# Performance work log

Measured on AMD Instinct MI355X. Metric: run time of the kernel, lower is better.

Reference implementation:

```python
import math
import jax, jax.numpy as jnp
import numpy as np

B, H, M, L, D, HID = 4, 8, 1024, 3200, 128, 1024
ATTN_LIM, RAMP = 2048, 128
PRE_DIV, LOSS_COEF = 16.0, 1e-06
SIZE = ATTN_LIM  # ExpireSpanDrop size = args.attn_lim


def skew(X, pad_value):
    # X: (BH, M, K) -> (BH, M, K+M), shifting row i right by i (relative-pos trick)
    BH, Mq, K = X.shape
    X = jnp.pad(X, ((0, 0), (0, 0), (0, Mq + 1)), constant_values=pad_value)
    X = X.reshape(BH, -1)[:, :-Mq]
    return X.reshape(BH, Mq, K + Mq)


def setup_inputs():
    key = jax.random.key(0)
    ks = jax.random.split(key, 6)
    query = jax.random.normal(ks[0], (B * H, M, D), jnp.float32)
    k = jax.random.normal(ks[1], (B * H, L, D), jnp.float32)
    v = jax.random.normal(ks[2], (B * H, L, D), jnp.float32)
    memory_hid = jax.random.normal(ks[3], (B, L, HID), jnp.float32)
    # age counters: oldest slot first; the current block (last M slots) goes down to -(M-1)
    memory_counter = jnp.broadcast_to(
        jnp.arange(L - 1, -1, -1, dtype=jnp.float32) - (M - 1), (B, L))
    key_pe = 0.02 * jax.random.normal(ks[4], (1, D, M), jnp.float32)
    span_w = 0.01 * jax.random.normal(ks[5], (1, HID), jnp.float32)
    span_b = jnp.full((1,), -math.log(1.0 / 0.1 - 1.0), jnp.float32)  # init_percentage=0.1
    return {"query": query, "key": k, "value": v, "memory_hid": memory_hid,
            "memory_counter": memory_counter, "key_pe": key_pe,
            "span_w": span_w, "span_b": span_b}


def reference(query, key, value, memory_hid, memory_counter, key_pe, span_w, span_b):
    max_mem = ATTN_LIM + M + RAMP
    # QK^T
    attn = jnp.einsum('bmd,bld->bml', query, key)                              # (BH, M, L)
    # --- ExpireSpanDrop (eval mode, no noise) ---
    max_span = jax.nn.sigmoid(
        jnp.einsum('blh,oh->blo', memory_hid / PRE_DIV, span_w)[..., 0] + span_b[0]) * SIZE  # (B, L)
    remaining_offset = max_span - memory_counter                               # (B, L)
    remaining_span = remaining_offset[:, None, :] - jnp.arange(M, dtype=jnp.float32)[None, :, None]  # (B, M, L)
    emask = jnp.clip(remaining_span / RAMP + 1.0, 0.0, 1.0)
    ramp_mask = ((emask > 0) & (emask < 1)).astype(emask.dtype)
    aux_loss = (remaining_span * ramp_mask).sum((-1, -2)) / RAMP / M * LOSS_COEF  # (B,)
    # causal mask (precomputed buffer in torch)
    causal = jnp.tril(jnp.ones((M, max_mem), jnp.float32), k=max_mem - M - 1)[:, -L:]
    mask = jnp.broadcast_to((emask * causal)[:, None], (B, H, M, L)).reshape(B * H, M, L)
    # --- relative position bias via skew ---
    attn_pos = skew(jnp.einsum('bmd,dk->bmk', query, key_pe[0]), 0.0)          # (BH, M, 2M)
    attn = attn.at[:, :, -2 * M:].add(attn_pos)
    # masked softmax + renormalization by soft mask
    attn = jnp.where(mask == 0, -jnp.inf, attn) / math.sqrt(D)
    attn = jax.nn.softmax(attn, axis=-1)
    attn = attn * mask
    attn = attn / (attn.sum(-1, keepdims=True) + 1e-08)
    out = jnp.einsum('bml,bld->bmd', attn, value)                              # (BH, M, D)
    return out, aux_loss, remaining_offset
```

## Files before the change

### kernel.cpp

```cpp
#include <hip/hip_runtime.h>
#include <stdint.h>

#define B_   4
#define H_   8
#define BH_  32
#define M_   1024
#define L_   3200
#define D_   128
#define HID_ 1024
#define NT64 50
#define CAUSAL_K 2175
#define POS_OFF  1152
#define SCALE 0.08838834764831845f
#define NEGV (-3.0e38f)
#define NEGH (-1.0e38f)

typedef short  bf16x8 __attribute__((ext_vector_type(8)));
typedef float  f32x4  __attribute__((ext_vector_type(4)));

__device__ __forceinline__ unsigned short f2bf(float x) {
    union { float f; uint32_t u; } v; v.f = x;
    return (unsigned short)((v.u + 0x7FFFu + ((v.u >> 16) & 1u)) >> 16);
}
__device__ __forceinline__ float bf2f(unsigned short h) {
    union { uint32_t u; float f; } v; v.u = ((uint32_t)h) << 16; return v.f;
}
__device__ __forceinline__ uint32_t pack_bf2(float lo, float hi) {
    union { float f; uint32_t u; } a, b; a.f = lo; b.f = hi;
    return __builtin_amdgcn_perm(b.u, a.u, 0x07060302u);
}

template <int CTRL>
__device__ __forceinline__ float dpp_movf(float x) {
    union { float f; int i; } u; u.f = x;
    u.i = __builtin_amdgcn_update_dpp(0, u.i, CTRL, 0xF, 0xF, true);
    return u.f;
}
__device__ __forceinline__ float row_max16(float x) {
    x = fmaxf(x, dpp_movf<0xB1>(x));
    x = fmaxf(x, dpp_movf<0x4E>(x));
    x = fmaxf(x, dpp_movf<0x141>(x));
    x = fmaxf(x, dpp_movf<0x140>(x));
    return x;
}
__device__ __forceinline__ float row_sum16(float x) {
    x += dpp_movf<0xB1>(x);
    x += dpp_movf<0x4E>(x);
    x += dpp_movf<0x141>(x);
    x += dpp_movf<0x140>(x);
    return x;
}

__global__ void span_pet_kernel(const float* __restrict__ hid,
                                const float* __restrict__ counter,
                                const float* __restrict__ sw,
                                const float* __restrict__ sb,
                                const float* __restrict__ PE,
                                float* __restrict__ r0_ws,
                                float* __restrict__ r0_out,
                                unsigned short* __restrict__ PET) {
    const int tid  = threadIdx.x;
    const int row  = blockIdx.x * 4 + (tid >> 6);
    const int lane = tid & 63;
    const float* h = hid + (size_t)row * HID_;
    float acc = 0.f;
#pragma unroll
    for (int it = 0; it < 4; ++it) {
        const int k = it * 256 + lane * 4;
        const float4 a = *(const float4*)(h + k);
        const float4 w = *(const float4*)(sw + k);
        acc += a.x*w.x + a.y*w.y + a.z*w.z + a.w*w.w;
    }
#pragma unroll
    for (int off = 32; off; off >>= 1) acc += __shfl_down(acc, off);
    if (lane == 0) {
        const float x  = acc * (1.0f/16.0f) + sb[0];
        const float ms = 2048.0f / (1.0f + __expf(-x));
        const float r0 = ms - counter[row];
        r0_ws[row]  = r0;
        r0_out[row] = r0;
    }
    if (PET != nullptr && blockIdx.x < M_ / 4) {
        const int c = blockIdx.x * 4 + (tid >> 6);
        const int e = tid & 63;
        const float lo = PE[(2*e)   * M_ + c];
        const float hi = PE[(2*e+1) * M_ + c];
        ((uint32_t*)PET)[c * 64 + e] = pack_bf2(lo, hi);
    }
}

__global__ void prep_kernel(const float* __restrict__ r0_ws,
                            float* __restrict__ tmax,
                            float* __restrict__ aux_out) {
    __shared__ float red[256];
    const int bid = blockIdx.x;
    const int tid = threadIdx.x;
    if (bid < 50) {
        const int wave = tid >> 6, lane = tid & 63;
        const int t = bid * 4 + wave;
        float v = r0_ws[t * 64 + lane];
#pragma unroll
        for (int off = 32; off; off >>= 1) v = fmaxf(v, __shfl_down(v, off));
        if (lane == 0) tmax[t] = v;
    } else {
        const int b = bid - 50;
        float s = 0.f;
        for (int l = tid; l < L_; l += 256) {
            const float r = r0_ws[b * L_ + l];
            const int fl = (int)floorf(r);
            int mlo = fl + 1;   if (mlo < 0) mlo = 0;
            int mhi = fl + 128; if (mhi > M_ - 1) mhi = M_ - 1;
            const int n = mhi - mlo + 1;
            if (n > 0) s += (float)n * r - 0.5f * (float)(mlo + mhi) * (float)n;
        }
        red[tid] = s; __syncthreads();
        for (int st = 128; st; st >>= 1) {
            if (tid < st) red[tid] += red[tid + st];
            __syncthreads();
        }
        if (tid == 0) aux_out[b] = red[0] * (1.0f/128.0f) * (1.0f/1024.0f) * 1e-6f;
    }
}

#define KS_STR 136
#define VT_STR 72
#define PE_STR 136
#define P_STR  72
#define T_STR  72

__global__ void __launch_bounds__(256, 2)
attn_kernel(const float* __restrict__ Q, const float* __restrict__ K,
            const float* __restrict__ V, const unsigned short* __restrict__ PET,
            const float* __restrict__ r0g, const float* __restrict__ tmax,
            float* __restrict__ out) {
    __shared__ short Ks[64 * KS_STR];
    __shared__ short Vt[128 * VT_STR];
    __shared__ short PEs[64 * PE_STR];
    __shared__ short Tb[2][64 * T_STR];
    __shared__ short Pb[64 * P_STR];

    const int flat = (int)blockIdx.x + 16 * (int)blockIdx.y;
    const int work = (flat & 7) * 64 + (flat >> 3);
    const int bh  = work >> 4;
    const int bxx = work & 15;
    const int b  = bh >> 3;
    const int i0 = bxx << 6;
    const int tid  = threadIdx.x;
    const int wave = tid >> 6;
    const int lane = tid & 63;
    const int lq   = lane & 15;
    const int quad = lane >> 4;
    const int lt_end = min(NT64, bxx + 35);

    const float live_thresh = (float)(i0 - 128);
    unsigned long long live_mask;
    {
        const int sidx = (lane < NT64) ? lane : (NT64 - 1);
        const float tv = tmax[b * NT64 + sidx];
        live_mask = __ballot((lane < NT64) && (lane < lt_end) && (tv > live_thresh));
    }
    auto next_live = [&](int s) -> int {
        const unsigned long long m = live_mask >> s;
        return m ? (s + __builtin_ctzll(m)) : lt_end;
    };

    float4 kp[8];
    float4 vpa[4], vpb[4];
    uint4  pep[4];
    float  rvp[4];
    float  rv[4];

    auto issue_prefetch = [&](int plt) {
        const int l0p = plt << 6;
        const float* kb = K + ((size_t)bh * L_ + l0p) * D_;
        const float* vb = V + ((size_t)bh * L_ + l0p) * D_;
#pragma unroll
        for (int it = 0; it < 8; ++it) {
            const int f = it * 256 + tid;
            kp[it] = *(const float4*)(kb + (f >> 5) * D_ + (f & 31) * 4);
        }
        const int p2 = (tid & 31) * 2;
#pragma unroll
        for (int it = 0; it < 4; ++it) {
            const int c = it * 8 + (tid >> 5);
            vpa[it] = *(const float4*)(vb + (size_t)p2 * D_ + c * 4);
            vpb[it] = *(const float4*)(vb + (size_t)(p2 + 1) * D_ + c * 4);
        }
        const int c0p = l0p - i0 - POS_OFF;
#pragma unroll
        for (int it = 0; it < 4; ++it) {
            const int f = it * 256 + tid;
            const int cg = c0p + (f >> 4);
            if ((unsigned)cg < (unsigned)M_)
                pep[it] = *(const uint4*)(PET + (size_t)cg * D_ + (f & 15) * 8);
            else { pep[it].x = 0; pep[it].y = 0; pep[it].z = 0; pep[it].w = 0; }
        }
        const float* rb = r0g + b * L_ + l0p;
#pragma unroll
        for (int nt = 0; nt < 4; ++nt) rvp[nt] = rb[nt * 16 + lq];
    };

    auto write_stage = [&]() {
#pragma unroll
        for (int it = 0; it < 8; ++it) {
            const int f = it * 256 + tid;
            uint2 w;
            w.x = pack_bf2(kp[it].x, kp[it].y);
            w.y = pack_bf2(kp[it].z, kp[it].w);
            *(uint2*)&Ks[(f >> 5) * KS_STR + (f & 31) * 4] = w;
        }
        const int p2 = (tid & 31) * 2;
#pragma unroll
        for (int it = 0; it < 4; ++it) {
            const int c = it * 8 + (tid >> 5);
            const float* a = (const float*)&vpa[it];
            const float* bb = (const float*)&vpb[it];
#pragma unroll
            for (int j = 0; j < 4; ++j)
                *(uint32_t*)&Vt[(c * 4 + j) * VT_STR + p2] = pack_bf2(a[j], bb[j]);
        }
#pragma unroll
        for (int it = 0; it < 4; ++it) {
            const int f = it * 256 + tid;
            *(uint4*)&PEs[(f >> 4) * PE_STR + (f & 15) * 8] = pep[it];
        }
#pragma unroll
        for (int nt = 0; nt < 4; ++nt) rv[nt] = rvp[nt];
    };

    int lt = next_live(0);
    if (lt < lt_end) issue_prefetch(lt);

    bf16x8 qfrag[4];
    {
        const float* qp = Q + ((size_t)bh * M_ + (i0 + wave * 16 + lq)) * D_;
#pragma unroll
        for (int kk = 0; kk < 4; ++kk) {
            const float4 q0 = *(const float4*)(qp + kk * 32 + quad * 8);
            const float4 q1 = *(const float4*)(qp + kk * 32 + quad * 8 + 4);
            union { bf16x8 v; uint32_t u[4]; } qq;
            qq.u[0] = pack_bf2(q0.x, q0.y); qq.u[1] = pack_bf2(q0.z, q0.w);
            qq.u[2] = pack_bf2(q1.x, q1.y); qq.u[3] = pack_bf2(q1.z, q1.w);
            qfrag[kk] = qq.v;
        }
    }

    auto computeT = [&](short* tb) {
        __builtin_amdgcn_s_setprio(1);
#pragma unroll
        for (int nt = 0; nt < 4; ++nt) {
            f32x4 acc = (f32x4){0.f, 0.f, 0.f, 0.f};
#pragma unroll
            for (int kk = 0; kk < 4; ++kk) {
                const bf16x8 bf = *(const bf16x8*)&PEs[(nt*16 + lq) * PE_STR + kk*32 + quad*8];
                acc = __builtin_amdgcn_mfma_f32_16x16x32_bf16(qfrag[kk], bf, acc, 0, 0, 0);
            }
#pragma unroll
            for (int r = 0; r < 4; ++r) {
                union { float f; uint32_t u; } t; t.f = acc[r];
                tb[(wave*16 + quad*4 + r) * T_STR + nt*16 + lq] = (short)(t.u >> 16);
            }
        }
        __builtin_amdgcn_s_setprio(0);
    };

    f32x4 oacc[8];
#pragma unroll
    for (int d = 0; d < 8; ++d) oacc[d] = (f32x4){0.f, 0.f, 0.f, 0.f};
    float mrun[4] = {NEGV, NEGV, NEGV, NEGV};
    float Zm[4]   = {0.f, 0.f, 0.f, 0.f};
    int tlo = 0, thi = 1;
    int prev_c0 = -(1 << 30);

    while (lt < lt_end) {
        const int l0 = lt << 6;
        const int c0 = l0 - i0 - POS_OFF;
        const bool need_pos = (c0 + 63 >= 0) && (c0 - 63 <= M_ - 1);
        const bool rolling  = need_pos && (prev_c0 == c0 - 64);

        __syncthreads();
        write_stage();
        __syncthreads();

        const int ltn = next_live(lt + 1);
        if (ltn < lt_end) issue_prefetch(ltn);

        f32x4 sfrag[4];
        __builtin_amdgcn_s_setprio(1);
#pragma unroll
        for (int nt = 0; nt < 4; ++nt) {
            f32x4 acc = (f32x4){0.f, 0.f, 0.f, 0.f};
#pragma unroll
            for (int kk = 0; kk < 4; ++kk) {
                const bf16x8 bf = *(const bf16x8*)&Ks[(nt*16 + lq) * KS_STR + kk*32 + quad*8];
                acc = __builtin_amdgcn_mfma_f32_16x16x32_bf16(qfrag[kk], bf, acc, 0, 0, 0);
            }
            sfrag[nt] = acc;
        }
        __builtin_amdgcn_s_setprio(0);

        if (need_pos) {
            if (rolling) {
                const int t = tlo; tlo = thi; thi = t;
                computeT(&Tb[thi][0]);
            } else {
                tlo = 0; thi = 1;
                computeT(&Tb[1][0]);
                uint4 lowp[4];
#pragma unroll
                for (int it = 0; it < 4; ++it) {
                    const int f = it * 256 + tid;
                    const int cg = (c0 - 64) + (f >> 4);
                    if ((unsigned)cg < (unsigned)M_)
                        lowp[it] = *(const uint4*)(PET + (size_t)cg * D_ + (f & 15) * 8);
                    else { lowp[it].x = 0; lowp[it].y = 0; lowp[it].z = 0; lowp[it].w = 0; }
                }
                __syncthreads();
#pragma unroll
                for (int it = 0; it < 4; ++it) {
                    const int f = it * 256 + tid;
                    *(uint4*)&PEs[(f >> 4) * PE_STR + (f & 15) * 8] = lowp[it];
                }
                __syncthreads();
                computeT(&Tb[0][0]);
            }
            prev_c0 = c0;
        } else {
            prev_c0 = -(1 << 30);
        }

#pragma unroll
        for (int r = 0; r < 4; ++r) {
            const int iq = i0 + wave*16 + quad*4 + r;
            const float fiq = (float)iq;
            float sv[4], ev[4];
#pragma unroll
            for (int nt = 0; nt < 4; ++nt) {
                const int l = l0 + nt*16 + lq;
                float s = sfrag[nt][r];
                const int c = l - iq - POS_OFF;
                if (need_pos && (unsigned)c < (unsigned)M_) {
                    const int cb = c - (c0 - 64);
                    const short* tbp = (cb & 64) ? &Tb[thi][0] : &Tb[tlo][0];
                    s += bf2f((unsigned short)tbp[(wave*16 + quad*4 + r) * T_STR + (cb & 63)]);
                }
                const float e = fminf(fmaxf((rv[nt] - fiq) * 0.0078125f + 1.0f, 0.f), 1.f);
                ev[nt] = e;
                const bool live = (l <= iq + CAUSAL_K) && (e > 0.f);
                sv[nt] = live ? s * SCALE : NEGV;
            }
            float v = fmaxf(fmaxf(sv[0], sv[1]), fmaxf(sv[2], sv[3]));
            v = row_max16(v);
            const float nm = fmaxf(mrun[r], v);
            float alpha = 1.f, pmsum = 0.f, pmv[4];
            if (nm > NEGH) {
                alpha = (mrun[r] > NEGH) ? __expf(mrun[r] - nm) : 0.f;
#pragma unroll
                for (int nt = 0; nt < 4; ++nt) {
                    const float p = __expf(sv[nt] - nm);
                    const float pm = p * ev[nt];
                    pmsum += pm; pmv[nt] = pm;
                }
            } else {
                pmv[0] = pmv[1] = pmv[2] = pmv[3] = 0.f;
            }
            pmsum = row_sum16(pmsum);
            mrun[r] = nm;
            Zm[r] = Zm[r] * alpha + pmsum;
#pragma unroll
            for (int d = 0; d < 8; ++d) oacc[d][r] *= alpha;
#pragma unroll
            for (int nt = 0; nt < 4; ++nt) {
                union { float f; uint32_t u; } t; t.f = pmv[nt];
                Pb[(wave*16 + quad*4 + r) * P_STR + nt*16 + lq] = (short)(t.u >> 16);
            }
        }

        __builtin_amdgcn_s_setprio(1);
#pragma unroll
        for (int kk = 0; kk < 2; ++kk) {
            const bf16x8 pf = *(const bf16x8*)&Pb[(wave*16 + lq) * P_STR + kk*32 + quad*8];
#pragma unroll
            for (int dt = 0; dt < 8; ++dt) {
                const bf16x8 vf = *(const bf16x8*)&Vt[(dt*16 + lq) * VT_STR + kk*32 + quad*8];
                oacc[dt] = __builtin_amdgcn_mfma_f32_16x16x32_bf16(pf, vf, oacc[dt], 0, 0, 0);
            }
        }
        __builtin_amdgcn_s_setprio(0);
        lt = ltn;
    }

#pragma unroll
    for (int r = 0; r < 4; ++r) {
        const int iq = i0 + wave*16 + quad*4 + r;
        const float inv = 1.0f / (Zm[r] + 1e-8f);
        float* op = out + ((size_t)bh * M_ + iq) * D_;
#pragma unroll
        for (int dt = 0; dt < 8; ++dt)
            op[dt*16 + lq] = oacc[dt][r] * inv;
    }
}

__global__ void __launch_bounds__(256, 2)
attn_fb_kernel(const float* __restrict__ Q, const float* __restrict__ K,
               const float* __restrict__ V, const float* __restrict__ PE,
               const float* __restrict__ r0g, const float* __restrict__ tmax,
               float* __restrict__ out) {
    __shared__ short Ks[64 * KS_STR];
    __shared__ short Vt[128 * VT_STR];
    __shared__ short PEP[64 * PE_STR];
    __shared__ short Tb[2][64 * T_STR];
    __shared__ float r0s[64];

    const int bh = blockIdx.y;
    const int b  = bh >> 3;
    const int i0 = blockIdx.x << 6;
    const int tid  = threadIdx.x;
    const int wave = tid >> 6;
    const int lane = tid & 63;
    const int lq   = lane & 15;
    const int quad = lane >> 4;

    bf16x8 qfrag[4];
    {
        const float* qp = Q + ((size_t)bh * M_ + (i0 + wave * 16 + lq)) * D_;
#pragma unroll
        for (int kk = 0; kk < 4; ++kk) {
            const float* p = qp + kk * 32 + quad * 8;
            bf16x8 f;
#pragma unroll
            for (int j = 0; j < 8; ++j) f[j] = (short)f2bf(p[j]);
            qfrag[kk] = f;
        }
    }

    f32x4 oacc[8];
#pragma unroll
    for (int d = 0; d < 8; ++d) oacc[d] = (f32x4){0.f, 0.f, 0.f, 0.f};
    float mrun[4] = {NEGV, NEGV, NEGV, NEGV};
    float Zr[4]   = {0.f, 0.f, 0.f, 0.f};
    float Zm[4]   = {0.f, 0.f, 0.f, 0.f};

    int tlo = 0, thi = 1;
    int prev_c0 = -100000;

    auto stagePE = [&](int cbase) {
#pragma unroll
        for (int it = 0; it < 8; ++it) {
            const int f4 = it * 256 + tid;
            const int d  = f4 >> 4;
            const int cl = (f4 & 15) << 2;
#pragma unroll
            for (int j = 0; j < 4; ++j) {
                const int cg = cbase + cl + j;
                const float v = (cg >= 0 && cg < M_) ? PE[d * M_ + cg] : 0.f;
                PEP[(cl + j) * PE_STR + d] = (short)f2bf(v);
            }
        }
    };
    auto computeT = [&](short* tb) {
#pragma unroll
        for (int nt = 0; nt < 4; ++nt) {
            f32x4 acc = (f32x4){0.f, 0.f, 0.f, 0.f};
#pragma unroll
            for (int kk = 0; kk < 4; ++kk) {
                const bf16x8 bf = *(const bf16x8*)&PEP[(nt*16 + lq) * PE_STR + kk*32 + quad*8];
                acc = __builtin_amdgcn_mfma_f32_16x16x32_bf16(qfrag[kk], bf, acc, 0, 0, 0);
            }
#pragma unroll
            for (int r = 0; r < 4; ++r)
                tb[(wave*16 + quad*4 + r) * T_STR + nt*16 + lq] = (short)f2bf(acc[r]);
        }
    };

    const int lt_end = min(NT64, (int)blockIdx.x + 35);
    for (int lt = 0; lt < lt_end; ++lt) {
        const int l0 = lt << 6;
        if (!(tmax[b * NT64 + lt] > (float)(i0 - 128))) continue;

        __syncthreads();
        {
            const float* kbase = K + ((size_t)bh * L_ + l0) * D_;
            const float* vbase = V + ((size_t)bh * L_ + l0) * D_;
#pragma unroll
            for (int it = 0; it < 8; ++it) {
                const int f4 = it * 256 + tid;
                const int row = f4 >> 5;
                const int ds  = (f4 & 31) << 2;
                const float4 kv = *(const float4*)(kbase + row * D_ + ds);
                uint2 pk;
                pk.x = (uint32_t)f2bf(kv.x) | ((uint32_t)f2bf(kv.y) << 16);
                pk.y = (uint32_t)f2bf(kv.z) | ((uint32_t)f2bf(kv.w) << 16);
                *(uint2*)&Ks[row * KS_STR + ds] = pk;
                const float4 vv = *(const float4*)(vbase + row * D_ + ds);
                Vt[(ds+0) * VT_STR + row] = (short)f2bf(vv.x);
                Vt[(ds+1) * VT_STR + row] = (short)f2bf(vv.y);
                Vt[(ds+2) * VT_STR + row] = (short)f2bf(vv.z);
                Vt[(ds+3) * VT_STR + row] = (short)f2bf(vv.w);
            }
            if (tid < 64) r0s[tid] = r0g[b * L_ + l0 + tid];
        }

        const int c0 = l0 - i0 - POS_OFF;
        const bool need_pos = (c0 + 63 >= 0) && (c0 - 63 <= M_ - 1);
        if (need_pos) {
            if (prev_c0 == c0 - 64) {
                const int t = tlo; tlo = thi; thi = t;
                stagePE(c0);
                __syncthreads();
                computeT(&Tb[thi][0]);
            } else {
                stagePE(c0 - 64);
                __syncthreads();
                computeT(&Tb[0][0]);
                __syncthreads();
                stagePE(c0);
                __syncthreads();
                computeT(&Tb[1][0]);
                tlo = 0; thi = 1;
            }
            prev_c0 = c0;
        } else {
            __syncthreads();
        }

        f32x4 sfrag[4];
#pragma unroll
        for (int nt = 0; nt < 4; ++nt) {
            f32x4 acc = (f32x4){0.f, 0.f, 0.f, 0.f};
#pragma unroll
            for (int kk = 0; kk < 4; ++kk) {
                const bf16x8 bf = *(const bf16x8*)&Ks[(nt*16 + lq) * KS_STR + kk*32 + quad*8];
                acc = __builtin_amdgcn_mfma_f32_16x16x32_bf16(qfrag[kk], bf, acc, 0, 0, 0);
            }
            sfrag[nt] = acc;
        }
        __syncthreads();

        float sv[4][4];
#pragma unroll
        for (int r = 0; r < 4; ++r) {
            const int iq = i0 + wave*16 + quad*4 + r;
#pragma unroll
            for (int nt = 0; nt < 4; ++nt) {
                const int l = l0 + nt*16 + lq;
                float s = sfrag[nt][r];
                const int c = l - iq - POS_OFF;
                if (c >= 0 && c < M_) {
                    const int cb = c - (c0 - 64);
                    const short* tbp = (cb & 64) ? &Tb[thi][0] : &Tb[tlo][0];
                    s += bf2f((unsigned short)tbp[(wave*16 + quad*4 + r) * T_STR + (cb & 63)]);
                }
                const float e = fminf(fmaxf((r0s[nt*16 + lq] - (float)iq) * 0.0078125f + 1.0f, 0.f), 1.f);
                const bool live = (l <= iq + CAUSAL_K) && (e > 0.f);
                sv[r][nt] = live ? s * SCALE : NEGV;
            }
        }

#pragma unroll
        for (int r = 0; r < 4; ++r) {
            float v = fmaxf(fmaxf(sv[r][0], sv[r][1]), fmaxf(sv[r][2], sv[r][3]));
            v = row_max16(v);
            const float nm = fmaxf(mrun[r], v);
            float alpha, pmv[4];
            float psum = 0.f, pmsum = 0.f;
            if (nm > NEGH) {
                alpha = (mrun[r] > NEGH) ? __expf(mrun[r] - nm) : 0.f;
                const int iq = i0 + wave*16 + quad*4 + r;
#pragma unroll
                for (int nt = 0; nt < 4; ++nt) {
                    const float p = __expf(sv[r][nt] - nm);
                    const float e = fminf(fmaxf((r0s[nt*16 + lq] - (float)iq) * 0.0078125f + 1.0f, 0.f), 1.f);
                    const float pm = p * e;
                    psum += p; pmsum += pm; pmv[nt] = pm;
                }
            } else {
                alpha = 1.f;
                pmv[0] = pmv[1] = pmv[2] = pmv[3] = 0.f;
            }
            psum  = row_sum16(psum);
            pmsum = row_sum16(pmsum);
            mrun[r] = nm;
            Zr[r] = Zr[r] * alpha + psum;
            Zm[r] = Zm[r] * alpha + pmsum;
#pragma unroll
            for (int d = 0; d < 8; ++d) oacc[d][r] *= alpha;
#pragma unroll
            for (int nt = 0; nt < 4; ++nt)
                PEP[(wave*16 + quad*4 + r) * P_STR + nt*16 + lq] = (short)f2bf(pmv[nt]);
        }
        __syncthreads();

#pragma unroll
        for (int kk = 0; kk < 2; ++kk) {
            const bf16x8 pf = *(const bf16x8*)&PEP[(wave*16 + lq) * P_STR + kk*32 + quad*8];
#pragma unroll
            for (int dt = 0; dt < 8; ++dt) {
                const bf16x8 vf = *(const bf16x8*)&Vt[(dt*16 + lq) * VT_STR + kk*32 + quad*8];
                oacc[dt] = __builtin_amdgcn_mfma_f32_16x16x32_bf16(pf, vf, oacc[dt], 0, 0, 0);
            }
        }
    }

#pragma unroll
    for (int r = 0; r < 4; ++r) {
        const int iq = i0 + wave*16 + quad*4 + r;
        const float inv = 1.0f / (Zm[r] + 1e-8f * Zr[r]);
        float* op = out + ((size_t)bh * M_ + iq) * D_;
#pragma unroll
        for (int dt = 0; dt < 8; ++dt)
            op[dt*16 + lq] = oacc[dt][r] * inv;
    }
}

extern "C" void kernel_launch(void* const* d_in, const int* in_sizes, int n_in,
                              void* d_out, int out_size, void* d_ws, size_t ws_size,
                              hipStream_t stream) {
    (void)in_sizes; (void)n_in; (void)out_size;
    const float* Q       = (const float*)d_in[0];
    const float* K       = (const float*)d_in[1];
    const float* V       = (const float*)d_in[2];
    const float* hid     = (const float*)d_in[3];
    const float* counter = (const float*)d_in[4];
    const float* pe      = (const float*)d_in[5];
    const float* sw      = (const float*)d_in[6];
    const float* sb      = (const float*)d_in[7];

    float* out    = (float*)d_out;
    float* aux    = out + (size_t)BH_ * M_ * D_;
    float* r0_out = aux + B_;

    float* r0_ws = (float*)d_ws;
    float* tmax  = r0_ws + B_ * L_;
    unsigned short* PET = (unsigned short*)(r0_ws + 13056);
    const bool use_pet = ws_size >= (size_t)(13056 * 4 + M_ * D_ * 2);

    span_pet_kernel<<<(B_ * L_) / 4, 256, 0, stream>>>(
        hid, counter, sw, sb, pe, r0_ws, r0_out, use_pet ? PET : nullptr);
    prep_kernel<<<54, 256, 0, stream>>>(r0_ws, tmax, aux);
    if (use_pet) {
        attn_kernel<<<dim3(M_ / 64, BH_), 256, 0, stream>>>(Q, K, V, PET, r0_ws, tmax, out);
    } else {
        attn_fb_kernel<<<dim3(M_ / 64, BH_), 256, 0, stream>>>(Q, K, V, pe, r0_ws, tmax, out);
    }
}
```

Baseline: 229.7 us.

## Split attention key tile across two wave groups with 512-thread blocks

The attention kernel grows from 256 to 512 threads. The two groups of four waves each handle half of every 64-key tile, for both QK and PV. Per-half softmax max and sum are exchanged through shared memory each tile, and the partial output accumulators are summed through shared memory at the end. The aim is more waves in flight and less per-wave MFMA and softmax work, to hide latency better. The cost is an extra barrier per tile, a final cross-group reduction, redundant position-bias computation in both groups, and a tighter register budget under the new launch bounds.

Result: slower. 255.8 us (+11.4%).

```diff
diff --git a/kernel.cpp b/kernel.cpp
--- a/kernel.cpp
+++ b/kernel.cpp
@@ -128,7 +128,7 @@
 #define P_STR  72
 #define T_STR  72
 
-__global__ void __launch_bounds__(256, 2)
+__global__ void __launch_bounds__(512, 2)
 attn_kernel(const float* __restrict__ Q, const float* __restrict__ K,
             const float* __restrict__ V, const unsigned short* __restrict__ PET,
             const float* __restrict__ r0g, const float* __restrict__ tmax,
@@ -147,6 +147,8 @@
     const int i0 = bxx << 6;
     const int tid  = threadIdx.x;
     const int wave = tid >> 6;
+    const int wr   = wave & 3;
+    const int wc   = wave >> 2;
     const int lane = tid & 63;
     const int lq   = lane & 15;
     const int quad = lane >> 4;
@@ -164,32 +166,32 @@
         return m ? (s + __builtin_ctzll(m)) : lt_end;
     };
 
-    float4 kp[8];
-    float4 vpa[4], vpb[4];
-    uint4  pep[4];
-    float  rvp[4];
-    float  rv[4];
+    float4 kp[4];
+    float4 vpa[2], vpb[2];
+    uint4  pep[2];
+    float  rvp[2];
+    float  rv[2];
 
     auto issue_prefetch = [&](int plt) {
         const int l0p = plt << 6;
         const float* kb = K + ((size_t)bh * L_ + l0p) * D_;
         const float* vb = V + ((size_t)bh * L_ + l0p) * D_;
 #pragma unroll
-        for (int it = 0; it < 8; ++it) {
-            const int f = it * 256 + tid;
+        for (int it = 0; it < 4; ++it) {
+            const int f = it * 512 + tid;
             kp[it] = *(const float4*)(kb + (f >> 5) * D_ + (f & 31) * 4);
         }
         const int p2 = (tid & 31) * 2;
 #pragma unroll
-        for (int it = 0; it < 4; ++it) {
-            const int c = it * 8 + (tid >> 5);
+        for (int it = 0; it < 2; ++it) {
+            const int c = it * 16 + (tid >> 5);
             vpa[it] = *(const float4*)(vb + (size_t)p2 * D_ + c * 4);
             vpb[it] = *(const float4*)(vb + (size_t)(p2 + 1) * D_ + c * 4);
         }
         const int c0p = l0p - i0 - POS_OFF;
 #pragma unroll
-        for (int it = 0; it < 4; ++it) {
-            const int f = it * 256 + tid;
+        for (int it = 0; it < 2; ++it) {
+            const int f = it * 512 + tid;
             const int cg = c0p + (f >> 4);
             if ((unsigned)cg < (unsigned)M_)
                 pep[it] = *(const uint4*)(PET + (size_t)cg * D_ + (f & 15) * 8);
@@ -197,13 +199,13 @@
         }
         const float* rb = r0g + b * L_ + l0p;
 #pragma unroll
-        for (int nt = 0; nt < 4; ++nt) rvp[nt] = rb[nt * 16 + lq];
+        for (int nt2 = 0; nt2 < 2; ++nt2) rvp[nt2] = rb[(wc * 2 + nt2) * 16 + lq];
     };
 
     auto write_stage = [&]() {
 #pragma unroll
-        for (int it = 0; it < 8; ++it) {
-            const int f = it * 256 + tid;
+        for (int it = 0; it < 4; ++it) {
+            const int f = it * 512 + tid;
             uint2 w;
             w.x = pack_bf2(kp[it].x, kp[it].y);
             w.y = pack_bf2(kp[it].z, kp[it].w);
@@ -211,8 +213,8 @@
         }
         const int p2 = (tid & 31) * 2;
 #pragma unroll
-        for (int it = 0; it < 4; ++it) {
-            const int c = it * 8 + (tid >> 5);
+        for (int it = 0; it < 2; ++it) {
+            const int c = it * 16 + (tid >> 5);
             const float* a = (const float*)&vpa[it];
             const float* bb = (const float*)&vpb[it];
 #pragma unroll
@@ -220,12 +222,12 @@
                 *(uint32_t*)&Vt[(c * 4 + j) * VT_STR + p2] = pack_bf2(a[j], bb[j]);
         }
 #pragma unroll
-        for (int it = 0; it < 4; ++it) {
-            const int f = it * 256 + tid;
+        for (int it = 0; it < 2; ++it) {
+            const int f = it * 512 + tid;
             *(uint4*)&PEs[(f >> 4) * PE_STR + (f & 15) * 8] = pep[it];
         }
 #pragma unroll
-        for (int nt = 0; nt < 4; ++nt) rv[nt] = rvp[nt];
+        for (int nt2 = 0; nt2 < 2; ++nt2) rv[nt2] = rvp[nt2];
     };
 
     int lt = next_live(0);
@@ -233,7 +235,7 @@
 
     bf16x8 qfrag[4];
     {
-        const float* qp = Q + ((size_t)bh * M_ + (i0 + wave * 16 + lq)) * D_;
+        const float* qp = Q + ((size_t)bh * M_ + (i0 + wr * 16 + lq)) * D_;
 #pragma unroll
         for (int kk = 0; kk < 4; ++kk) {
             const float4 q0 = *(const float4*)(qp + kk * 32 + quad * 8);
@@ -258,7 +260,7 @@
 #pragma unroll
             for (int r = 0; r < 4; ++r) {
                 union { float f; uint32_t u; } t; t.f = acc[r];
-                tb[(wave*16 + quad*4 + r) * T_STR + nt*16 + lq] = (short)(t.u >> 16);
+                tb[(wr*16 + quad*4 + r) * T_STR + nt*16 + lq] = (short)(t.u >> 16);
             }
         }
         __builtin_amdgcn_s_setprio(0);
@@ -285,17 +287,18 @@
         const int ltn = next_live(lt + 1);
         if (ltn < lt_end) issue_prefetch(ltn);
 
-        f32x4 sfrag[4];
+        f32x4 sfrag[2];
         __builtin_amdgcn_s_setprio(1);
 #pragma unroll
-        for (int nt = 0; nt < 4; ++nt) {
+        for (int nt2 = 0; nt2 < 2; ++nt2) {
+            const int nt = wc * 2 + nt2;
             f32x4 acc = (f32x4){0.f, 0.f, 0.f, 0.f};
 #pragma unroll
             for (int kk = 0; kk < 4; ++kk) {
                 const bf16x8 bf = *(const bf16x8*)&Ks[(nt*16 + lq) * KS_STR + kk*32 + quad*8];
                 acc = __builtin_amdgcn_mfma_f32_16x16x32_bf16(qfrag[kk], bf, acc, 0, 0, 0);
             }
-            sfrag[nt] = acc;
+            sfrag[nt2] = acc;
         }
         __builtin_amdgcn_s_setprio(0);
 
@@ -306,10 +309,10 @@
             } else {
                 tlo = 0; thi = 1;
                 computeT(&Tb[1][0]);
-                uint4 lowp[4];
-#pragma unroll
-                for (int it = 0; it < 4; ++it) {
-                    const int f = it * 256 + tid;
+                uint4 lowp[2];
+#pragma unroll
+                for (int it = 0; it < 2; ++it) {
+                    const int f = it * 512 + tid;
                     const int cg = (c0 - 64) + (f >> 4);
                     if ((unsigned)cg < (unsigned)M_)
                         lowp[it] = *(const uint4*)(PET + (size_t)cg * D_ + (f & 15) * 8);
@@ -317,8 +320,8 @@
                 }
                 __syncthreads();
 #pragma unroll
-                for (int it = 0; it < 4; ++it) {
-                    const int f = it * 256 + tid;
+                for (int it = 0; it < 2; ++it) {
+                    const int f = it * 512 + tid;
                     *(uint4*)&PEs[(f >> 4) * PE_STR + (f & 15) * 8] = lowp[it];
                 }
                 __syncthreads();
@@ -329,60 +332,70 @@
             prev_c0 = -(1 << 30);
         }
 
+        float pmv[4][2];
 #pragma unroll
         for (int r = 0; r < 4; ++r) {
-            const int iq = i0 + wave*16 + quad*4 + r;
+            const int iq = i0 + wr*16 + quad*4 + r;
             const float fiq = (float)iq;
-            float sv[4], ev[4];
-#pragma unroll
-            for (int nt = 0; nt < 4; ++nt) {
+            float sv[2], ev[2];
+#pragma unroll
+            for (int nt2 = 0; nt2 < 2; ++nt2) {
+                const int nt = wc*2 + nt2;
                 const int l = l0 + nt*16 + lq;
-                float s = sfrag[nt][r];
+                float s = sfrag[nt2][r];
                 const int c = l - iq - POS_OFF;
                 if (need_pos && (unsigned)c < (unsigned)M_) {
                     const int cb = c - (c0 - 64);
                     const short* tbp = (cb & 64) ? &Tb[thi][0] : &Tb[tlo][0];
-                    s += bf2f((unsigned short)tbp[(wave*16 + quad*4 + r) * T_STR + (cb & 63)]);
+                    s += bf2f((unsigned short)tbp[(wr*16 + quad*4 + r) * T_STR + (cb & 63)]);
                 }
-                const float e = fminf(fmaxf((rv[nt] - fiq) * 0.0078125f + 1.0f, 0.f), 1.f);
-                ev[nt] = e;
+                const float e = fminf(fmaxf((rv[nt2] - fiq) * 0.0078125f + 1.0f, 0.f), 1.f);
+                ev[nt2] = e;
                 const bool live = (l <= iq + CAUSAL_K) && (e > 0.f);
-                sv[nt] = live ? s * SCALE : NEGV;
-            }
-            float v = fmaxf(fmaxf(sv[0], sv[1]), fmaxf(sv[2], sv[3]));
-            v = row_max16(v);
-            const float nm = fmaxf(mrun[r], v);
-            float alpha = 1.f, pmsum = 0.f, pmv[4];
+                sv[nt2] = live ? s * SCALE : NEGV;
+            }
+            float lm = fmaxf(sv[0], sv[1]);
+            lm = row_max16(lm);
+            const float p0 = __expf(sv[0] - lm);
+            const float p1 = __expf(sv[1] - lm);
+            const float pm0 = p0 * ev[0], pm1 = p1 * ev[1];
+            const float pms = row_sum16(pm0 + pm1);
+            pmv[r][0] = pm0; pmv[r][1] = pm1;
+            if (lq == 0) {
+                float2 st; st.x = lm; st.y = pms;
+                *(float2*)((float*)&Pb[(wr*16 + quad*4 + r) * P_STR + 64] + wc*2) = st;
+            }
+        }
+        __syncthreads();
+
+#pragma unroll
+        for (int r = 0; r < 4; ++r) {
+            const int row = wr*16 + quad*4 + r;
+            const float4 st = *(const float4*)&Pb[row * P_STR + 64];
+            const float nm = fmaxf(mrun[r], fmaxf(st.x, st.z));
+            float w0, w1;
             if (nm > NEGH) {
-                alpha = (mrun[r] > NEGH) ? __expf(mrun[r] - nm) : 0.f;
-#pragma unroll
-                for (int nt = 0; nt < 4; ++nt) {
-                    const float p = __expf(sv[nt] - nm);
-                    const float pm = p * ev[nt];
-                    pmsum += pm; pmv[nt] = pm;
-                }
-            } else {
-                pmv[0] = pmv[1] = pmv[2] = pmv[3] = 0.f;
-            }
-            pmsum = row_sum16(pmsum);
-            mrun[r] = nm;
-            Zm[r] = Zm[r] * alpha + pmsum;
-#pragma unroll
-            for (int d = 0; d < 8; ++d) oacc[d][r] *= alpha;
-#pragma unroll
-            for (int nt = 0; nt < 4; ++nt) {
-                union { float f; uint32_t u; } t; t.f = pmv[nt];
-                Pb[(wave*16 + quad*4 + r) * P_STR + nt*16 + lq] = (short)(t.u >> 16);
-            }
+                const float alpha = __expf(mrun[r] - nm);
+                const float cf0   = __expf(st.x - nm);
+                const float cf1   = __expf(st.z - nm);
+                Zm[r] = Zm[r] * alpha + st.y * cf0 + st.w * cf1;
+                mrun[r] = nm;
+#pragma unroll
+                for (int d = 0; d < 8; ++d) oacc[d][r] *= alpha;
+                const float cw = wc ? cf1 : cf0;
+                w0 = pmv[r][0] * cw; w1 = pmv[r][1] * cw;
+            } else { w0 = 0.f; w1 = 0.f; }
+            union { float f; uint32_t u; } t0, t1; t0.f = w0; t1.f = w1;
+            Pb[row * P_STR + (wc*2 + 0)*16 + lq] = (short)(t0.u >> 16);
+            Pb[row * P_STR + (wc*2 + 1)*16 + lq] = (short)(t1.u >> 16);
         }
 
         __builtin_amdgcn_s_setprio(1);
-#pragma unroll
-        for (int kk = 0; kk < 2; ++kk) {
-            const bf16x8 pf = *(const bf16x8*)&Pb[(wave*16 + lq) * P_STR + kk*32 + quad*8];
+        {
+            const bf16x8 pf = *(const bf16x8*)&Pb[(wr*16 + lq) * P_STR + wc*32 + quad*8];
 #pragma unroll
             for (int dt = 0; dt < 8; ++dt) {
-                const bf16x8 vf = *(const bf16x8*)&Vt[(dt*16 + lq) * VT_STR + kk*32 + quad*8];
+                const bf16x8 vf = *(const bf16x8*)&Vt[(dt*16 + lq) * VT_STR + wc*32 + quad*8];
                 oacc[dt] = __builtin_amdgcn_mfma_f32_16x16x32_bf16(pf, vf, oacc[dt], 0, 0, 0);
             }
         }
@@ -390,14 +403,33 @@
         lt = ltn;
     }
 
-#pragma unroll
-    for (int r = 0; r < 4; ++r) {
-        const int iq = i0 + wave*16 + quad*4 + r;
-        const float inv = 1.0f / (Zm[r] + 1e-8f);
-        float* op = out + ((size_t)bh * M_ + iq) * D_;
-#pragma unroll
-        for (int dt = 0; dt < 8; ++dt)
-            op[dt*16 + lq] = oacc[dt][r] * inv;
+    __syncthreads();
+    float* EP = (float*)PEs;
+#pragma unroll
+    for (int half = 0; half < 2; ++half) {
+        if (wc == 1) {
+#pragma unroll
+            for (int d2 = 0; d2 < 4; ++d2) {
+                const int dt = half*4 + d2;
+#pragma unroll
+                for (int r = 0; r < 4; ++r)
+                    EP[(wr*16 + quad*4 + r) * 64 + d2*16 + lq] = oacc[dt][r];
+            }
+        }
+        __syncthreads();
+        if (wc == 0) {
+#pragma unroll
+            for (int d2 = 0; d2 < 4; ++d2) {
+                const int dt = half*4 + d2;
+#pragma unroll
+                for (int r = 0; r < 4; ++r) {
+                    const int iq = i0 + wr*16 + quad*4 + r;
+                    const float v = oacc[dt][r] + EP[(wr*16 + quad*4 + r) * 64 + d2*16 + lq];
+                    out[((size_t)bh * M_ + iq) * D_ + dt*16 + lq] = v / (Zm[r] + 1e-8f);
+                }
+            }
+        }
+        __syncthreads();
     }
 }
 
@@ -639,7 +671,7 @@
         hid, counter, sw, sb, pe, r0_ws, r0_out, use_pet ? PET : nullptr);
     prep_kernel<<<54, 256, 0, stream>>>(r0_ws, tmax, aux);
     if (use_pet) {
-        attn_kernel<<<dim3(M_ / 64, BH_), 256, 0, stream>>>(Q, K, V, PET, r0_ws, tmax, out);
+        attn_kernel<<<dim3(M_ / 64, BH_), 512, 0, stream>>>(Q, K, V, PET, r0_ws, tmax, out);
     } else {
         attn_fb_kernel<<<dim3(M_ / 64, BH_), 256, 0, stream>>>(Q, K, V, pe, r0_ws, tmax, out);
     }
```
